# Optimization experiments

Measured on AMD Instinct MI355X. Metric: run time of the kernel, lower is better.

Reference implementation:

```python
import jax, jax.numpy as jnp
import numpy as np

B, N, H, W = 8, 16384, 64, 64
CTX, OUT, ST = 32, 2, 1
HID = [516, 256, 128, 64, 32, 16]
IN_SIZE = CTX + 2 + ST + OUT  # 37


def _bilinear_sample(img, coord):
    """torch F.grid_sample, mode=bilinear, padding=zeros, align_corners=False.
    img: [B,C,H,W]; coord: [B,N,2] (x,y in [-1,1]). Returns [B,C,N]."""
    _, _, Hh, Ww = img.shape
    gx = (coord[..., 0] + 1.0) * (Ww * 0.5) - 0.5
    gy = (coord[..., 1] + 1.0) * (Hh * 0.5) - 0.5
    x0 = jnp.floor(gx)
    y0 = jnp.floor(gy)
    wx1 = gx - x0
    wy1 = gy - y0

    def tap(xi, yi, w):
        valid = (xi >= 0) & (xi < Ww) & (yi >= 0) & (yi < Hh)
        xc = jnp.clip(xi, 0, Ww - 1).astype(jnp.int32)
        yc = jnp.clip(yi, 0, Hh - 1).astype(jnp.int32)
        vals = jax.vmap(lambda im, y, x: im[:, y, x])(img, yc, xc)  # [B,C,N]
        return vals * (w * valid)[:, None, :]

    return (tap(x0, y0, (1 - wx1) * (1 - wy1))
            + tap(x0 + 1, y0, wx1 * (1 - wy1))
            + tap(x0, y0 + 1, (1 - wx1) * wy1)
            + tap(x0 + 1, y0 + 1, wx1 * wy1))


def _layer_shapes():
    shapes = [(IN_SIZE, HID[0])]
    for i in range(len(HID) - 1):
        shapes.append((HID[i] + IN_SIZE, HID[i + 1]))
    shapes.append((HID[-1], OUT))
    return shapes


def setup_inputs():
    key = jax.random.key(0)
    ks = jax.random.split(key, 4 + 7)
    inp = {
        "lr_fields": jax.random.normal(ks[0], (B, OUT, H, W), jnp.float32),
        "context_grid": jax.random.normal(ks[1], (B, CTX, H, W), jnp.float32),
        "hr_eps": jax.random.normal(ks[2], (B, H, W), jnp.float32),
        "coord": jax.random.uniform(ks[3], (B, N, 2), jnp.float32, -1.0, 1.0),
    }
    for j, (fi, fo) in enumerate(_layer_shapes()):
        inp[f"W{j}"] = jax.random.normal(ks[4 + j], (fi, fo), jnp.float32) / np.sqrt(fi)
        inp[f"b{j}"] = jnp.zeros((fo,), jnp.float32)
    return inp


def reference(lr_fields, context_grid, hr_eps, coord,
              W0, b0, W1, b1, W2, b2, W3, b3, W4, b4, W5, b5, W6, b6):
    # original permutes (0,1,3,2) before grid_sample -> swap spatial axes
    ctx_pts = _bilinear_sample(jnp.swapaxes(context_grid, 2, 3), coord)  # [B,CTX,N]
    lr_pts = _bilinear_sample(jnp.swapaxes(lr_fields, 2, 3), coord)      # [B,OUT,N]
    eps_pts = _bilinear_sample(jnp.swapaxes(hr_eps[:, None], 2, 3), coord)  # [B,1,N]
    x_in = jnp.concatenate([
        jnp.transpose(ctx_pts, (0, 2, 1)),
        coord,
        jnp.transpose(lr_pts, (0, 2, 1)),
        jnp.transpose(eps_pts, (0, 2, 1)),
    ], axis=2)  # [B,N,37]
    x = jax.nn.relu(x_in @ W0 + b0)
    for Wl, bl in ((W1, b1), (W2, b2), (W3, b3), (W4, b4), (W5, b5)):
        x = jax.nn.relu(jnp.concatenate([x, x_in], axis=2) @ Wl + bl)
    return x @ W6 + b6  # [B,N,2]
```

## Files before the change

### kernel.cpp

```cpp
#include <hip/hip_runtime.h>


#define NTH     1024
#define NWAVES  16
#define MPTS    32
#define MTILES  (MPTS / 16)
#define SROW    872
#define XIN_OFF 0
#define HA_OFF  64
#define HB_OFF  608
#define NPOINTS (8 * 16384)
#define GRIDX   (NPOINTS / MPTS)
#define LDSBYTES (MPTS * SROW * 2)

typedef short          short8 __attribute__((ext_vector_type(8)));
typedef float          f32x4  __attribute__((ext_vector_type(4)));
typedef unsigned short u16;

__device__ __forceinline__ u16 f2bf(float f) {
    unsigned int u = __builtin_bit_cast(unsigned int, f);
    u += 0x7fffu + ((u >> 16) & 1u);
    return (u16)(u >> 16);
}

__constant__ int pk_base8[8] = {0, 4224, 23680, 28800, 30336, 30848, 31040, 31104};
__constant__ int pk_ks[7]    = {2, 19, 10, 6, 4, 3, 1};
__constant__ int pk_khp[7]   = {0, 544, 256, 128, 64, 32, 32};
__constant__ int pk_kact[7]  = {0, 516, 256, 128, 64, 32, 16};
__constant__ int pk_nact[7]  = {516, 256, 128, 64, 32, 16, 2};

struct WPtrs { const float* W[7]; };

__global__ void pack_weights(WPtrs wp, u16* __restrict__ out)
{
    const int f = blockIdx.x * blockDim.x + threadIdx.x;
    if (f >= 31104) return;
    int l = 0;
    while (l < 6 && f >= pk_base8[l + 1]) ++l;
    const int r    = f - pk_base8[l];
    const int lane = r & 63;
    const int t    = r >> 6;
    const int ks   = pk_ks[l];
    const int s    = t % ks;
    const int nt   = t / ks;
    const int n    = nt * 16 + (lane & 15);
    const int k0   = s * 32 + (lane >> 4) * 8;
    const int nact = pk_nact[l];
    const int khp  = pk_khp[l];
    const int kact = pk_kact[l];
    const float* W = wp.W[l];

    union { short8 v; u16 e[8]; } frag;
#pragma unroll
    for (int j = 0; j < 8; ++j) {
        const int k = k0 + j;
        float v = 0.0f;
        if (n < nact) {
            if (k < khp) {
                if (k < kact) v = W[k * nact + n];
            } else {
                const int xr = k - khp;
                if (xr < 37) v = W[(kact + xr) * nact + n];
            }
        }
        frag.e[j] = f2bf(v);
    }
    *(short8*)(out + (size_t)f * 8) = frag.v;
}

template<int KHP, int HSEG, int OSEG, int NT, int NG, int MS, int NACT,
         int LBASE, bool XIN, bool RELU, bool GOUT>
__device__ __forceinline__ void mlayer(const u16* __restrict__ wpack,
                                       const float* __restrict__ bias,
                                       u16* __restrict__ s_act,
                                       float* __restrict__ gout, int p0,
                                       int wave, int lane)
{
    constexpr int KHS   = KHP / 32;
    constexpr int KS    = KHS + (XIN ? 2 : 0);
    constexpr int NGRP  = (NT + NG - 1) / NG;
    constexpr int MGRP  = MTILES / MS;
    constexpr int UNITS = NGRP * MGRP;
    const int lm = lane & 15;
    const int lq = lane >> 4;
    const u16* wbase = wpack + LBASE + lane * 8;

    for (int u = wave; u < UNITS; u += NWAVES) {
        const int gn = u % NGRP;
        const int gm = u / NGRP;
        const int n0 = gn * NG;
        const int m0 = gm * MS;

        const u16* arow[MS];
#pragma unroll
        for (int m = 0; m < MS; ++m)
            arow[m] = s_act + ((m0 + m) * 16 + lm) * SROW + lq * 8;

        f32x4 acc[NG][MS];
#pragma unroll
        for (int t = 0; t < NG; ++t)
#pragma unroll
            for (int m = 0; m < MS; ++m)
                acc[t][m] = (f32x4){0.f, 0.f, 0.f, 0.f};

#pragma unroll
        for (int s = 0; s < KS; ++s) {
            const int ab = (s < KHS) ? (HSEG + s * 32)
                                     : (XIN_OFF + (s - KHS) * 32);
            short8 a[MS];
#pragma unroll
            for (int m = 0; m < MS; ++m)
                a[m] = *(const short8*)(arow[m] + ab);
#pragma unroll
            for (int t = 0; t < NG; ++t) {
                const int nt = n0 + t;
                if ((NT % NG) && nt >= NT) break;
                const short8 b = *(const short8*)(wbase + (size_t)(nt * KS + s) * 512);
#pragma unroll
                for (int m = 0; m < MS; ++m)
                    acc[t][m] = __builtin_amdgcn_mfma_f32_16x16x32_bf16(a[m], b, acc[t][m], 0, 0, 0);
            }
        }

#pragma unroll
        for (int t = 0; t < NG; ++t) {
            const int nt = n0 + t;
            if ((NT % NG) && nt >= NT) break;
            const int n = nt * 16 + lm;
            const float bv = (n < NACT) ? bias[n] : 0.f;
#pragma unroll
            for (int m = 0; m < MS; ++m) {
#pragma unroll
                for (int r = 0; r < 4; ++r) {
                    float v = acc[t][m][r] + bv;
                    if (RELU) v = fmaxf(v, 0.f);
                    const int pt = (m0 + m) * 16 + lq * 4 + r;
                    if (GOUT) {
                        if (n < NACT)
                            gout[(size_t)(p0 + pt) * 2 + n] = v;
                    } else {
                        s_act[pt * SROW + OSEG + n] = f2bf(v);
                    }
                }
            }
        }
    }
}

struct MainParams {
    const float* lr;
    const float* ctx;
    const float* eps;
    const float* coord;
    const float* Bb[7];
    const u16*   wpack;
    float*       out;
};

__global__ __launch_bounds__(NTH, 8)
void cont_decoder_mfma(MainParams p)
{
    extern __shared__ u16 s_act[];
    __shared__ int   s_x0[MPTS], s_y0[MPTS];
    __shared__ float s_wx[MPTS], s_wy[MPTS];

    const int tid  = threadIdx.x;
    const int wave = tid >> 6;
    const int lane = tid & 63;
    const int p0   = blockIdx.x * MPTS;
    const int b    = p0 >> 14;

    for (int i = tid; i < MPTS * 43; i += NTH) {
        const int pt = i / 43, c = i % 43;
        const int col = (c < 27) ? (37 + c) : (592 + (c - 27));
        s_act[pt * SROW + col] = 0;
    }

    if (tid < MPTS) {
        const int pt = p0 + tid;
        const float cx = p.coord[2 * pt];
        const float cy = p.coord[2 * pt + 1];
        const float gx = (cx + 1.0f) * 32.0f - 0.5f;
        const float gy = (cy + 1.0f) * 32.0f - 0.5f;
        const float fx0 = floorf(gx), fy0 = floorf(gy);
        s_x0[tid] = (int)fx0;
        s_y0[tid] = (int)fy0;
        s_wx[tid] = gx - fx0;
        s_wy[tid] = gy - fy0;
        s_act[tid * SROW + 32] = f2bf(cx);
        s_act[tid * SROW + 33] = f2bf(cy);
    }
    __syncthreads();

    for (int idx = tid; idx < MPTS * 35; idx += NTH) {
        const int t = idx / 35;
        const int c = idx % 35;
        const float* base;
        int col;
        if (c < 32)      { base = p.ctx + (size_t)(b * 32 + c) * 4096;       col = c; }
        else if (c < 34) { base = p.lr  + (size_t)(b * 2 + (c - 32)) * 4096; col = 34 + (c - 32); }
        else             { base = p.eps + (size_t)b * 4096;                   col = 36; }

        const int   x0 = s_x0[t], y0 = s_y0[t];
        const float wx = s_wx[t], wy = s_wy[t];
        const int x1 = x0 + 1, y1 = y0 + 1;
        const bool xv0 = (x0 >= 0) & (x0 < 64);
        const bool xv1 = (x1 >= 0) & (x1 < 64);
        const bool yv0 = (y0 >= 0) & (y0 < 64);
        const bool yv1 = (y1 >= 0) & (y1 < 64);
        const int xc0 = min(max(x0, 0), 63), xc1 = min(max(x1, 0), 63);
        const int yc0 = min(max(y0, 0), 63), yc1 = min(max(y1, 0), 63);

        const float w00 = (1.0f - wx) * (1.0f - wy) * ((xv0 && yv0) ? 1.0f : 0.0f);
        const float w10 = wx * (1.0f - wy)          * ((xv1 && yv0) ? 1.0f : 0.0f);
        const float w01 = (1.0f - wx) * wy          * ((xv0 && yv1) ? 1.0f : 0.0f);
        const float w11 = wx * wy                   * ((xv1 && yv1) ? 1.0f : 0.0f);

        const float val = w00 * base[xc0 * 64 + yc0]
                        + w10 * base[xc1 * 64 + yc0]
                        + w01 * base[xc0 * 64 + yc1]
                        + w11 * base[xc1 * 64 + yc1];
        s_act[t * SROW + col] = f2bf(val);
    }
    __syncthreads();

    mlayer<  0,  HA_OFF, HA_OFF, 33, 1, 2, 516, 0,      true,  true,  false>(p.wpack, p.Bb[0], s_act, nullptr, p0, wave, lane);
    __syncthreads();
    mlayer<544,  HA_OFF, HB_OFF, 16, 1, 2, 256, 33792,  true,  true,  false>(p.wpack, p.Bb[1], s_act, nullptr, p0, wave, lane);
    __syncthreads();
    mlayer<256,  HB_OFF, HA_OFF,  8, 1, 2, 128, 189440, true,  true,  false>(p.wpack, p.Bb[2], s_act, nullptr, p0, wave, lane);
    __syncthreads();
    mlayer<128,  HA_OFF, HB_OFF,  4, 1, 2,  64, 230400, true,  true,  false>(p.wpack, p.Bb[3], s_act, nullptr, p0, wave, lane);
    __syncthreads();
    mlayer< 64,  HB_OFF, HA_OFF,  2, 1, 2,  32, 242688, true,  true,  false>(p.wpack, p.Bb[4], s_act, nullptr, p0, wave, lane);
    __syncthreads();
    mlayer< 32,  HA_OFF, HB_OFF,  1, 1, 2,  16, 246784, true,  true,  false>(p.wpack, p.Bb[5], s_act, nullptr, p0, wave, lane);
    __syncthreads();
    mlayer< 32,  HB_OFF, 0,       1, 1, 2,   2, 248320, false, false, true >(p.wpack, p.Bb[6], s_act, p.out,   p0, wave, lane);
}

extern "C" void kernel_launch(void* const* d_in, const int* in_sizes, int n_in,
                              void* d_out, int out_size, void* d_ws, size_t ws_size,
                              hipStream_t stream)
{
    WPtrs wp;
    for (int l = 0; l < 7; ++l) wp.W[l] = (const float*)d_in[4 + 2 * l];

    MainParams p;
    p.lr    = (const float*)d_in[0];
    p.ctx   = (const float*)d_in[1];
    p.eps   = (const float*)d_in[2];
    p.coord = (const float*)d_in[3];
    for (int l = 0; l < 7; ++l) p.Bb[l] = (const float*)d_in[5 + 2 * l];
    p.wpack = (const u16*)d_ws;
    p.out   = (float*)d_out;

    hipFuncSetAttribute((const void*)cont_decoder_mfma,
                        hipFuncAttributeMaxDynamicSharedMemorySize, LDSBYTES);

    hipLaunchKernelGGL(pack_weights, dim3(122), dim3(256), 0, stream, wp, (u16*)d_ws);
    hipLaunchKernelGGL(cont_decoder_mfma, dim3(GRIDX), dim3(NTH), LDSBYTES, stream, p);
}
```

Baseline: 217.8 us.

## Software-pipeline MFMA operand loads and run tail layers per-wave without block barriers

The layer routine drops the NG grouping and gives each wave one N-tile. It prefetches A fragments (double-buffered) and B weight fragments (three deep) ahead of the MFMAs, so load latency overlaps with compute. The last four small layers now run on only two waves, each owning a 16-point row slice, with no __syncthreads between them. This removes four block-wide barriers, but leaves those layers serialized on two waves while the other 14 idle and raises register pressure from the prefetch buffers.

```diff
diff --git a/kernel.cpp b/kernel.cpp
--- a/kernel.cpp
+++ b/kernel.cpp
@@ -68,83 +68,78 @@
     *(short8*)(out + (size_t)f * 8) = frag.v;
 }
 
-template<int KHP, int HSEG, int OSEG, int NT, int NG, int MS, int NACT,
-         int LBASE, bool XIN, bool RELU, bool GOUT>
+template<int KHP, int HSEG, int OSEG, int NT, int MS, int NACT,
+         int LBASE, int NWV, bool XIN, bool RELU, bool GOUT>
 __device__ __forceinline__ void mlayer(const u16* __restrict__ wpack,
                                        const float* __restrict__ bias,
                                        u16* __restrict__ s_act,
                                        float* __restrict__ gout, int p0,
                                        int wave, int lane)
 {
-    constexpr int KHS   = KHP / 32;
-    constexpr int KS    = KHS + (XIN ? 2 : 0);
-    constexpr int NGRP  = (NT + NG - 1) / NG;
-    constexpr int MGRP  = MTILES / MS;
-    constexpr int UNITS = NGRP * MGRP;
+    constexpr int KHS = KHP / 32;
+    constexpr int KS  = KHS + (XIN ? 2 : 0);
     const int lm = lane & 15;
     const int lq = lane >> 4;
     const u16* wbase = wpack + LBASE + lane * 8;
 
-    for (int u = wave; u < UNITS; u += NWAVES) {
-        const int gn = u % NGRP;
-        const int gm = u / NGRP;
-        const int n0 = gn * NG;
-        const int m0 = gm * MS;
-
+#define AB(s) (((s) < KHS) ? (HSEG + (s) * 32) : (XIN_OFF + ((s) - KHS) * 32))
+
+    for (int u = wave; u < NT; u += NWV) {
+        const int nt = u;
         const u16* arow[MS];
 #pragma unroll
         for (int m = 0; m < MS; ++m)
-            arow[m] = s_act + ((m0 + m) * 16 + lm) * SROW + lq * 8;
-
-        f32x4 acc[NG][MS];
-#pragma unroll
-        for (int t = 0; t < NG; ++t)
+            arow[m] = s_act + (m * 16 + lm) * SROW + lq * 8;
+        const u16* bptr = wbase + (size_t)nt * KS * 512;
+
+        f32x4 acc[MS];
+#pragma unroll
+        for (int m = 0; m < MS; ++m)
+            acc[m] = (f32x4){0.f, 0.f, 0.f, 0.f};
+
+        short8 br[3];
+        short8 ar[2][MS];
+        br[0] = *(const short8*)(bptr);
+#pragma unroll
+        for (int m = 0; m < MS; ++m)
+            ar[0][m] = *(const short8*)(arow[m] + AB(0));
+        if constexpr (KS >= 2) br[1] = *(const short8*)(bptr + 512);
+        if constexpr (KS >= 3) br[2] = *(const short8*)(bptr + 1024);
+
+#pragma unroll
+        for (int s = 0; s < KS; ++s) {
+            if (s + 1 < KS) {
+#pragma unroll
+                for (int m = 0; m < MS; ++m)
+                    ar[(s + 1) & 1][m] = *(const short8*)(arow[m] + AB(s + 1));
+            }
+            const short8 b = br[s % 3];
+            if (s + 3 < KS)
+                br[s % 3] = *(const short8*)(bptr + (size_t)(s + 3) * 512);
 #pragma unroll
             for (int m = 0; m < MS; ++m)
-                acc[t][m] = (f32x4){0.f, 0.f, 0.f, 0.f};
-
-#pragma unroll
-        for (int s = 0; s < KS; ++s) {
-            const int ab = (s < KHS) ? (HSEG + s * 32)
-                                     : (XIN_OFF + (s - KHS) * 32);
-            short8 a[MS];
-#pragma unroll
-            for (int m = 0; m < MS; ++m)
-                a[m] = *(const short8*)(arow[m] + ab);
-#pragma unroll
-            for (int t = 0; t < NG; ++t) {
-                const int nt = n0 + t;
-                if ((NT % NG) && nt >= NT) break;
-                const short8 b = *(const short8*)(wbase + (size_t)(nt * KS + s) * 512);
-#pragma unroll
-                for (int m = 0; m < MS; ++m)
-                    acc[t][m] = __builtin_amdgcn_mfma_f32_16x16x32_bf16(a[m], b, acc[t][m], 0, 0, 0);
-            }
+                acc[m] = __builtin_amdgcn_mfma_f32_16x16x32_bf16(ar[s & 1][m], b, acc[m], 0, 0, 0);
         }
 
-#pragma unroll
-        for (int t = 0; t < NG; ++t) {
-            const int nt = n0 + t;
-            if ((NT % NG) && nt >= NT) break;
-            const int n = nt * 16 + lm;
-            const float bv = (n < NACT) ? bias[n] : 0.f;
-#pragma unroll
-            for (int m = 0; m < MS; ++m) {
-#pragma unroll
-                for (int r = 0; r < 4; ++r) {
-                    float v = acc[t][m][r] + bv;
-                    if (RELU) v = fmaxf(v, 0.f);
-                    const int pt = (m0 + m) * 16 + lq * 4 + r;
-                    if (GOUT) {
-                        if (n < NACT)
-                            gout[(size_t)(p0 + pt) * 2 + n] = v;
-                    } else {
-                        s_act[pt * SROW + OSEG + n] = f2bf(v);
-                    }
+        const int n = nt * 16 + lm;
+        const float bv = (n < NACT) ? bias[n] : 0.f;
+#pragma unroll
+        for (int m = 0; m < MS; ++m) {
+#pragma unroll
+            for (int r = 0; r < 4; ++r) {
+                float v = acc[m][r] + bv;
+                if (RELU) v = fmaxf(v, 0.f);
+                const int pt = m * 16 + lq * 4 + r;
+                if (GOUT) {
+                    if (n < NACT)
+                        gout[(size_t)(p0 + pt) * 2 + n] = v;
+                } else {
+                    s_act[pt * SROW + OSEG + n] = f2bf(v);
                 }
             }
         }
     }
+#undef AB
 }
 
 struct MainParams {
@@ -224,19 +219,21 @@
     }
     __syncthreads();
 
-    mlayer<  0,  HA_OFF, HA_OFF, 33, 1, 2, 516, 0,      true,  true,  false>(p.wpack, p.Bb[0], s_act, nullptr, p0, wave, lane);
-    __syncthreads();
-    mlayer<544,  HA_OFF, HB_OFF, 16, 1, 2, 256, 33792,  true,  true,  false>(p.wpack, p.Bb[1], s_act, nullptr, p0, wave, lane);
-    __syncthreads();
-    mlayer<256,  HB_OFF, HA_OFF,  8, 1, 2, 128, 189440, true,  true,  false>(p.wpack, p.Bb[2], s_act, nullptr, p0, wave, lane);
-    __syncthreads();
-    mlayer<128,  HA_OFF, HB_OFF,  4, 1, 2,  64, 230400, true,  true,  false>(p.wpack, p.Bb[3], s_act, nullptr, p0, wave, lane);
-    __syncthreads();
-    mlayer< 64,  HB_OFF, HA_OFF,  2, 1, 2,  32, 242688, true,  true,  false>(p.wpack, p.Bb[4], s_act, nullptr, p0, wave, lane);
-    __syncthreads();
-    mlayer< 32,  HA_OFF, HB_OFF,  1, 1, 2,  16, 246784, true,  true,  false>(p.wpack, p.Bb[5], s_act, nullptr, p0, wave, lane);
-    __syncthreads();
-    mlayer< 32,  HB_OFF, 0,       1, 1, 2,   2, 248320, false, false, true >(p.wpack, p.Bb[6], s_act, p.out,   p0, wave, lane);
+    mlayer<  0,  HA_OFF, HA_OFF, 33, 2, 516, 0,      NWAVES, true,  true,  false>(p.wpack, p.Bb[0], s_act, nullptr, p0, wave, lane);
+    __syncthreads();
+    mlayer<544,  HA_OFF, HB_OFF, 16, 2, 256, 33792,  NWAVES, true,  true,  false>(p.wpack, p.Bb[1], s_act, nullptr, p0, wave, lane);
+    __syncthreads();
+    mlayer<256,  HB_OFF, HA_OFF,  8, 2, 128, 189440, NWAVES, true,  true,  false>(p.wpack, p.Bb[2], s_act, nullptr, p0, wave, lane);
+    __syncthreads();
+
+    if (wave < MTILES) {
+        u16* sb = s_act + wave * 16 * SROW;
+        const int pp = p0 + wave * 16;
+        mlayer<128, HA_OFF, HB_OFF, 4, 1,  64, 230400, 1, true,  true,  false>(p.wpack, p.Bb[3], sb, nullptr, pp, 0, lane);
+        mlayer< 64, HB_OFF, HA_OFF, 2, 1,  32, 242688, 1, true,  true,  false>(p.wpack, p.Bb[4], sb, nullptr, pp, 0, lane);
+        mlayer< 32, HA_OFF, HB_OFF, 1, 1,  16, 246784, 1, true,  true,  false>(p.wpack, p.Bb[5], sb, nullptr, pp, 0, lane);
+        mlayer< 32, HB_OFF, 0,      1, 1,   2, 248320, 1, false, false, true >(p.wpack, p.Bb[6], sb, p.out,  pp, 0, lane);
+    }
 }
 
 extern "C" void kernel_launch(void* const* d_in, const int* in_sizes, int n_in,
```

Result: no change. 220.7 us (+1.3%).

## Restructure MLP layer MFMA tiling with swapped operands and chunked weight loads

Applied to the files above, without the earlier changes.

Rewrites the per-layer MFMA routine so each wave owns a fixed M half (mg) and strides over N tiles by 8, replacing the old dynamic unit loop. The MFMA operands are swapped (weights as A, activations as B) so each lane holds four consecutive output columns, which allows vectorized short4 stores to LDS, float4 bias loads and float2 global output writes. K steps are processed in chunks of 5, batching the activation and weight fragment loads ahead of the MFMAs to expose more memory-level parallelism. In exchange, per-wave register use rises and the per-wave work split across layers changes.

```diff
diff --git a/kernel.cpp b/kernel.cpp
--- a/kernel.cpp
+++ b/kernel.cpp
@@ -14,6 +14,7 @@
 #define LDSBYTES (MPTS * SROW * 2)
 
 typedef short          short8 __attribute__((ext_vector_type(8)));
+typedef short          short4v __attribute__((ext_vector_type(4)));
 typedef float          f32x4  __attribute__((ext_vector_type(4)));
 typedef unsigned short u16;
 
@@ -68,81 +69,93 @@
     *(short8*)(out + (size_t)f * 8) = frag.v;
 }
 
-template<int KHP, int HSEG, int OSEG, int NT, int NG, int MS, int NACT,
-         int LBASE, bool XIN, bool RELU, bool GOUT>
+template<int KHP, int HSEG, int OSEG, int NT, int NACT, int LBASE,
+         bool XIN, bool RELU, bool GOUT>
 __device__ __forceinline__ void mlayer(const u16* __restrict__ wpack,
                                        const float* __restrict__ bias,
                                        u16* __restrict__ s_act,
                                        float* __restrict__ gout, int p0,
                                        int wave, int lane)
 {
-    constexpr int KHS   = KHP / 32;
-    constexpr int KS    = KHS + (XIN ? 2 : 0);
-    constexpr int NGRP  = (NT + NG - 1) / NG;
-    constexpr int MGRP  = MTILES / MS;
-    constexpr int UNITS = NGRP * MGRP;
+    constexpr int KHS  = KHP / 32;
+    constexpr int KS   = KHS + (XIN ? 2 : 0);
+    constexpr int UMAX = (NT + 7) / 8;
+    constexpr int CK   = 5;
     const int lm = lane & 15;
     const int lq = lane >> 4;
-    const u16* wbase = wpack + LBASE + lane * 8;
-
-    for (int u = wave; u < UNITS; u += NWAVES) {
-        const int gn = u % NGRP;
-        const int gm = u / NGRP;
-        const int n0 = gn * NG;
-        const int m0 = gm * MS;
-
-        const u16* arow[MS];
-#pragma unroll
-        for (int m = 0; m < MS; ++m)
-            arow[m] = s_act + ((m0 + m) * 16 + lm) * SROW + lq * 8;
-
-        f32x4 acc[NG][MS];
-#pragma unroll
-        for (int t = 0; t < NG; ++t)
-#pragma unroll
-            for (int m = 0; m < MS; ++m)
-                acc[t][m] = (f32x4){0.f, 0.f, 0.f, 0.f};
-
-#pragma unroll
-        for (int s = 0; s < KS; ++s) {
-            const int ab = (s < KHS) ? (HSEG + s * 32)
-                                     : (XIN_OFF + (s - KHS) * 32);
-            short8 a[MS];
-#pragma unroll
-            for (int m = 0; m < MS; ++m)
-                a[m] = *(const short8*)(arow[m] + ab);
-#pragma unroll
-            for (int t = 0; t < NG; ++t) {
-                const int nt = n0 + t;
-                if ((NT % NG) && nt >= NT) break;
-                const short8 b = *(const short8*)(wbase + (size_t)(nt * KS + s) * 512);
-#pragma unroll
-                for (int m = 0; m < MS; ++m)
-                    acc[t][m] = __builtin_amdgcn_mfma_f32_16x16x32_bf16(a[m], b, acc[t][m], 0, 0, 0);
-            }
-        }
-
-#pragma unroll
-        for (int t = 0; t < NG; ++t) {
-            const int nt = n0 + t;
-            if ((NT % NG) && nt >= NT) break;
-            const int n = nt * 16 + lm;
-            const float bv = (n < NACT) ? bias[n] : 0.f;
-#pragma unroll
-            for (int m = 0; m < MS; ++m) {
-#pragma unroll
-                for (int r = 0; r < 4; ++r) {
-                    float v = acc[t][m][r] + bv;
-                    if (RELU) v = fmaxf(v, 0.f);
-                    const int pt = (m0 + m) * 16 + lq * 4 + r;
-                    if (GOUT) {
-                        if (n < NACT)
-                            gout[(size_t)(p0 + pt) * 2 + n] = v;
-                    } else {
-                        s_act[pt * SROW + OSEG + n] = f2bf(v);
-                    }
-                }
-            }
+    const int mg = wave & 1;
+    const int ng = (wave >> 1) & 7;
+
+    if (NT < 8 && ng >= NT) return;
+
+    const u16* arow = s_act + (mg * 16 + lm) * SROW + lq * 8;
+    const u16* wl   = wpack + LBASE + lane * 8;
+
+    f32x4 acc[UMAX];
+#pragma unroll
+    for (int u = 0; u < UMAX; ++u)
+        acc[u] = (f32x4){0.f, 0.f, 0.f, 0.f};
+
+#pragma unroll
+    for (int kc = 0; kc < KS; kc += CK) {
+        short8 a[CK];
+#pragma unroll
+        for (int j = 0; j < CK; ++j) {
+            const int s = kc + j;
+            if (s < KS) {
+                const int ab = (s < KHS) ? (HSEG + s * 32)
+                                         : (XIN_OFF + (s - KHS) * 32);
+                a[j] = *(const short8*)(arow + ab);
+            }
+        }
+#pragma unroll
+        for (int u = 0; u < UMAX; ++u) {
+            const int nt = ng + 8 * u;
+            if (nt < NT) {
+                const u16* bp = wl + (size_t)(nt * KS + kc) * 512;
+                short8 bf[CK];
+#pragma unroll
+                for (int j = 0; j < CK; ++j)
+                    if (kc + j < KS)
+                        bf[j] = *(const short8*)(bp + (size_t)j * 512);
+#pragma unroll
+                for (int j = 0; j < CK; ++j)
+                    if (kc + j < KS)
+                        acc[u] = __builtin_amdgcn_mfma_f32_16x16x32_bf16(bf[j], a[j], acc[u], 0, 0, 0);
+            }
+        }
+    }
+
+#pragma unroll
+    for (int u = 0; u < UMAX; ++u) {
+        const int nt = ng + 8 * u;
+        if (nt >= NT) continue;
+        const int bn = nt * 16 + lq * 4;
+        float bv[4];
+        if (bn + 4 <= NACT) {
+            const f32x4 b4 = *(const f32x4*)(bias + bn);
+            bv[0] = b4[0]; bv[1] = b4[1]; bv[2] = b4[2]; bv[3] = b4[3];
+        } else {
+#pragma unroll
+            for (int r = 0; r < 4; ++r)
+                bv[r] = (bn + r < NACT) ? bias[bn + r] : 0.f;
+        }
+        if (GOUT) {
+            if (lq == 0) {
+                float2 o;
+                o.x = acc[u][0] + bv[0];
+                o.y = acc[u][1] + bv[1];
+                *(float2*)(gout + (size_t)(p0 + mg * 16 + lm) * 2) = o;
+            }
+        } else {
+            short4v o;
+#pragma unroll
+            for (int r = 0; r < 4; ++r) {
+                float v = acc[u][r] + bv[r];
+                if (RELU) v = fmaxf(v, 0.f);
+                o[r] = (short)f2bf(v);
+            }
+            *(short4v*)(s_act + (size_t)(mg * 16 + lm) * SROW + OSEG + bn) = o;
         }
     }
 }
@@ -224,19 +237,19 @@
     }
     __syncthreads();
 
-    mlayer<  0,  HA_OFF, HA_OFF, 33, 1, 2, 516, 0,      true,  true,  false>(p.wpack, p.Bb[0], s_act, nullptr, p0, wave, lane);
-    __syncthreads();
-    mlayer<544,  HA_OFF, HB_OFF, 16, 1, 2, 256, 33792,  true,  true,  false>(p.wpack, p.Bb[1], s_act, nullptr, p0, wave, lane);
-    __syncthreads();
-    mlayer<256,  HB_OFF, HA_OFF,  8, 1, 2, 128, 189440, true,  true,  false>(p.wpack, p.Bb[2], s_act, nullptr, p0, wave, lane);
-    __syncthreads();
-    mlayer<128,  HA_OFF, HB_OFF,  4, 1, 2,  64, 230400, true,  true,  false>(p.wpack, p.Bb[3], s_act, nullptr, p0, wave, lane);
-    __syncthreads();
-    mlayer< 64,  HB_OFF, HA_OFF,  2, 1, 2,  32, 242688, true,  true,  false>(p.wpack, p.Bb[4], s_act, nullptr, p0, wave, lane);
-    __syncthreads();
-    mlayer< 32,  HA_OFF, HB_OFF,  1, 1, 2,  16, 246784, true,  true,  false>(p.wpack, p.Bb[5], s_act, nullptr, p0, wave, lane);
-    __syncthreads();
-    mlayer< 32,  HB_OFF, 0,       1, 1, 2,   2, 248320, false, false, true >(p.wpack, p.Bb[6], s_act, p.out,   p0, wave, lane);
+    mlayer<  0,  HA_OFF, HA_OFF, 33, 516, 0,      true,  true,  false>(p.wpack, p.Bb[0], s_act, nullptr, p0, wave, lane);
+    __syncthreads();
+    mlayer<544,  HA_OFF, HB_OFF, 16, 256, 33792,  true,  true,  false>(p.wpack, p.Bb[1], s_act, nullptr, p0, wave, lane);
+    __syncthreads();
+    mlayer<256,  HB_OFF, HA_OFF,  8, 128, 189440, true,  true,  false>(p.wpack, p.Bb[2], s_act, nullptr, p0, wave, lane);
+    __syncthreads();
+    mlayer<128,  HA_OFF, HB_OFF,  4,  64, 230400, true,  true,  false>(p.wpack, p.Bb[3], s_act, nullptr, p0, wave, lane);
+    __syncthreads();
+    mlayer< 64,  HB_OFF, HA_OFF,  2,  32, 242688, true,  true,  false>(p.wpack, p.Bb[4], s_act, nullptr, p0, wave, lane);
+    __syncthreads();
+    mlayer< 32,  HA_OFF, HB_OFF,  1,  16, 246784, true,  true,  false>(p.wpack, p.Bb[5], s_act, nullptr, p0, wave, lane);
+    __syncthreads();
+    mlayer< 32,  HB_OFF, 0,       1,   2, 248320, false, false, true >(p.wpack, p.Bb[6], s_act, p.out,   p0, wave, lane);
 }
 
 extern "C" void kernel_launch(void* const* d_in, const int* in_sizes, int n_in,
```

After: 262.6 us. 1.21x slower.

## Swap MFMA operands for transposed output and assign contiguous N-tiles per wave

Applied to the files above, without the earlier changes.

Swaps the MFMA A/B operands so each lane's accumulator holds four consecutive output features of one point. This allows vectorized bias loads and packed 4-wide bf16 LDS stores, plus float2 global output stores. The work split changes from strided units to a fixed block of UPW N-tiles per wave, with weight fragments prefetched before the MFMA burst and s_setprio raised around it. Layer 0 becomes unbalanced (3 tiles on some waves, 33 tiles over 16 waves), and idle waves now return early.

```diff
diff --git a/kernel.cpp b/kernel.cpp
--- a/kernel.cpp
+++ b/kernel.cpp
@@ -13,8 +13,9 @@
 #define GRIDX   (NPOINTS / MPTS)
 #define LDSBYTES (MPTS * SROW * 2)
 
-typedef short          short8 __attribute__((ext_vector_type(8)));
-typedef float          f32x4  __attribute__((ext_vector_type(4)));
+typedef short          short8  __attribute__((ext_vector_type(8)));
+typedef short          short4v __attribute__((ext_vector_type(4)));
+typedef float          f32x4   __attribute__((ext_vector_type(4)));
 typedef unsigned short u16;
 
 __device__ __forceinline__ u16 f2bf(float f) {
@@ -68,80 +69,96 @@
     *(short8*)(out + (size_t)f * 8) = frag.v;
 }
 
-template<int KHP, int HSEG, int OSEG, int NT, int NG, int MS, int NACT,
-         int LBASE, bool XIN, bool RELU, bool GOUT>
+template<int KHP, int HSEG, int OSEG, int NT, int UPW, int NACT, int LBASE,
+         bool XIN, bool RELU, bool GOUT>
 __device__ __forceinline__ void mlayer(const u16* __restrict__ wpack,
                                        const float* __restrict__ bias,
                                        u16* __restrict__ s_act,
                                        float* __restrict__ gout, int p0,
                                        int wave, int lane)
 {
-    constexpr int KHS   = KHP / 32;
-    constexpr int KS    = KHS + (XIN ? 2 : 0);
-    constexpr int NGRP  = (NT + NG - 1) / NG;
-    constexpr int MGRP  = MTILES / MS;
-    constexpr int UNITS = NGRP * MGRP;
+    constexpr int KHS = KHP / 32;
+    constexpr int KS  = KHS + (XIN ? 2 : 0);
+    constexpr int MS  = MTILES;
     const int lm = lane & 15;
     const int lq = lane >> 4;
-    const u16* wbase = wpack + LBASE + lane * 8;
-
-    for (int u = wave; u < UNITS; u += NWAVES) {
-        const int gn = u % NGRP;
-        const int gm = u / NGRP;
-        const int n0 = gn * NG;
-        const int m0 = gm * MS;
-
-        const u16* arow[MS];
+
+    const int n0 = wave * UPW;
+    if (n0 >= NT) return;
+
+    const u16* arow[MS];
+#pragma unroll
+    for (int m = 0; m < MS; ++m)
+        arow[m] = s_act + (m * 16 + lm) * SROW + lq * 8;
+    const u16* wl = wpack + LBASE + lane * 8;
+
+    f32x4 acc[UPW][MS];
+#pragma unroll
+    for (int i = 0; i < UPW; ++i)
 #pragma unroll
         for (int m = 0; m < MS; ++m)
-            arow[m] = s_act + ((m0 + m) * 16 + lm) * SROW + lq * 8;
-
-        f32x4 acc[NG][MS];
-#pragma unroll
-        for (int t = 0; t < NG; ++t)
-#pragma unroll
-            for (int m = 0; m < MS; ++m)
-                acc[t][m] = (f32x4){0.f, 0.f, 0.f, 0.f};
-
-#pragma unroll
-        for (int s = 0; s < KS; ++s) {
-            const int ab = (s < KHS) ? (HSEG + s * 32)
-                                     : (XIN_OFF + (s - KHS) * 32);
-            short8 a[MS];
-#pragma unroll
-            for (int m = 0; m < MS; ++m)
-                a[m] = *(const short8*)(arow[m] + ab);
-#pragma unroll
-            for (int t = 0; t < NG; ++t) {
-                const int nt = n0 + t;
-                if ((NT % NG) && nt >= NT) break;
-                const short8 b = *(const short8*)(wbase + (size_t)(nt * KS + s) * 512);
+            acc[i][m] = (f32x4){0.f, 0.f, 0.f, 0.f};
+
+#pragma unroll
+    for (int s = 0; s < KS; ++s) {
+        const int ab = (s < KHS) ? (HSEG + s * 32)
+                                 : (XIN_OFF + (s - KHS) * 32);
+        short8 a[MS];
+#pragma unroll
+        for (int m = 0; m < MS; ++m)
+            a[m] = *(const short8*)(arow[m] + ab);
+
+        short8 bfr[UPW];
+#pragma unroll
+        for (int i = 0; i < UPW; ++i)
+            if (n0 + i < NT)
+                bfr[i] = *(const short8*)(wl + (size_t)((n0 + i) * KS + s) * 512);
+
+        __builtin_amdgcn_s_setprio(1);
+#pragma unroll
+        for (int i = 0; i < UPW; ++i)
+            if (n0 + i < NT)
 #pragma unroll
                 for (int m = 0; m < MS; ++m)
-                    acc[t][m] = __builtin_amdgcn_mfma_f32_16x16x32_bf16(a[m], b, acc[t][m], 0, 0, 0);
+                    acc[i][m] = __builtin_amdgcn_mfma_f32_16x16x32_bf16(bfr[i], a[m], acc[i][m], 0, 0, 0);
+        __builtin_amdgcn_s_setprio(0);
+    }
+
+#pragma unroll
+    for (int i = 0; i < UPW; ++i) {
+        const int nt = n0 + i;
+        if (nt >= NT) continue;
+        const int bn = nt * 16 + lq * 4;
+        float bv[4];
+        if (bn + 4 <= NACT) {
+            const f32x4 b4 = *(const f32x4*)(bias + bn);
+            bv[0] = b4[0]; bv[1] = b4[1]; bv[2] = b4[2]; bv[3] = b4[3];
+        } else {
+#pragma unroll
+            for (int r = 0; r < 4; ++r)
+                bv[r] = (bn + r < NACT) ? bias[bn + r] : 0.f;
+        }
+        if (GOUT) {
+            if (lq == 0) {
+#pragma unroll
+                for (int m = 0; m < MS; ++m) {
+                    float2 o;
+                    o.x = acc[i][m][0] + bv[0];
+                    o.y = acc[i][m][1] + bv[1];
+                    *(float2*)(gout + (size_t)(p0 + m * 16 + lm) * 2) = o;
+                }
             }
-        }
-
-#pragma unroll
-        for (int t = 0; t < NG; ++t) {
-            const int nt = n0 + t;
-            if ((NT % NG) && nt >= NT) break;
-            const int n = nt * 16 + lm;
-            const float bv = (n < NACT) ? bias[n] : 0.f;
+        } else {
 #pragma unroll
             for (int m = 0; m < MS; ++m) {
+                short4v o;
 #pragma unroll
                 for (int r = 0; r < 4; ++r) {
-                    float v = acc[t][m][r] + bv;
+                    float v = acc[i][m][r] + bv[r];
                     if (RELU) v = fmaxf(v, 0.f);
-                    const int pt = (m0 + m) * 16 + lq * 4 + r;
-                    if (GOUT) {
-                        if (n < NACT)
-                            gout[(size_t)(p0 + pt) * 2 + n] = v;
-                    } else {
-                        s_act[pt * SROW + OSEG + n] = f2bf(v);
-                    }
+                    o[r] = (short)f2bf(v);
                 }
+                *(short4v*)(s_act + (size_t)(m * 16 + lm) * SROW + OSEG + bn) = o;
             }
         }
     }
@@ -224,19 +241,19 @@
     }
     __syncthreads();
 
-    mlayer<  0,  HA_OFF, HA_OFF, 33, 1, 2, 516, 0,      true,  true,  false>(p.wpack, p.Bb[0], s_act, nullptr, p0, wave, lane);
-    __syncthreads();
-    mlayer<544,  HA_OFF, HB_OFF, 16, 1, 2, 256, 33792,  true,  true,  false>(p.wpack, p.Bb[1], s_act, nullptr, p0, wave, lane);
-    __syncthreads();
-    mlayer<256,  HB_OFF, HA_OFF,  8, 1, 2, 128, 189440, true,  true,  false>(p.wpack, p.Bb[2], s_act, nullptr, p0, wave, lane);
-    __syncthreads();
-    mlayer<128,  HA_OFF, HB_OFF,  4, 1, 2,  64, 230400, true,  true,  false>(p.wpack, p.Bb[3], s_act, nullptr, p0, wave, lane);
-    __syncthreads();
-    mlayer< 64,  HB_OFF, HA_OFF,  2, 1, 2,  32, 242688, true,  true,  false>(p.wpack, p.Bb[4], s_act, nullptr, p0, wave, lane);
-    __syncthreads();
-    mlayer< 32,  HA_OFF, HB_OFF,  1, 1, 2,  16, 246784, true,  true,  false>(p.wpack, p.Bb[5], s_act, nullptr, p0, wave, lane);
-    __syncthreads();
-    mlayer< 32,  HB_OFF, 0,       1, 1, 2,   2, 248320, false, false, true >(p.wpack, p.Bb[6], s_act, p.out,   p0, wave, lane);
+    mlayer<  0,  HA_OFF, HA_OFF, 33, 3, 516, 0,      true,  true,  false>(p.wpack, p.Bb[0], s_act, nullptr, p0, wave, lane);
+    __syncthreads();
+    mlayer<544,  HA_OFF, HB_OFF, 16, 2, 256, 33792,  true,  true,  false>(p.wpack, p.Bb[1], s_act, nullptr, p0, wave, lane);
+    __syncthreads();
+    mlayer<256,  HB_OFF, HA_OFF,  8, 1, 128, 189440, true,  true,  false>(p.wpack, p.Bb[2], s_act, nullptr, p0, wave, lane);
+    __syncthreads();
+    mlayer<128,  HA_OFF, HB_OFF,  4, 1,  64, 230400, true,  true,  false>(p.wpack, p.Bb[3], s_act, nullptr, p0, wave, lane);
+    __syncthreads();
+    mlayer< 64,  HB_OFF, HA_OFF,  2, 1,  32, 242688, true,  true,  false>(p.wpack, p.Bb[4], s_act, nullptr, p0, wave, lane);
+    __syncthreads();
+    mlayer< 32,  HA_OFF, HB_OFF,  1, 1,  16, 246784, true,  true,  false>(p.wpack, p.Bb[5], s_act, nullptr, p0, wave, lane);
+    __syncthreads();
+    mlayer< 32,  HB_OFF, 0,       1, 1,   2, 248320, false, false, true >(p.wpack, p.Bb[6], s_act, p.out,   p0, wave, lane);
 }
 
 extern "C" void kernel_launch(void* const* d_in, const int* in_sizes, int n_in,
```

Measured after the change: 231.1 us. 1.06x slower.
